# Optimization experiments

Measured on AMD Instinct MI355X. Metric: run time of the kernel, lower is better.

## Reference

```python
import jax, jax.numpy as jnp
import numpy as np

N, E, IN, H, OUT = 50000, 800000, 256, 128, 64


def setup_inputs() -> dict:
    key = jax.random.key(0)
    ks = jax.random.split(key, 4)
    x = jax.random.normal(ks[0], (N, IN), dtype=jnp.float32)
    edge_index = jax.random.randint(ks[1], (2, E), 0, N, dtype=jnp.int64)
    W1 = jax.random.normal(ks[2], (IN, H), dtype=jnp.float32) / np.float32(np.sqrt(IN))
    b1 = jnp.zeros((H,), jnp.float32)
    W2 = jax.random.normal(ks[3], (H, OUT), dtype=jnp.float32) / np.float32(np.sqrt(H))
    b2 = jnp.zeros((OUT,), jnp.float32)
    return {"x": x, "edge_index": edge_index, "W1": W1, "b1": b1, "W2": W2, "b2": b2}


def _gcn_conv(x, W, b, src, dst, norm, n):
    # PyG GCNConv: linear transform, then symmetric-normalized aggregation, then bias
    h = x @ W                                        # [n, d_out]
    agg = jax.ops.segment_sum(h[src] * norm[:, None], dst, num_segments=n)
    return agg + b


def reference(x, edge_index, W1, b1, W2, b2):
    n = x.shape[0]
    loop = jnp.arange(n, dtype=edge_index.dtype)
    # add self-loops (GCNConv default add_self_loops=True)
    src = jnp.concatenate([edge_index[0], loop])
    dst = jnp.concatenate([edge_index[1], loop])
    # symmetric normalization deg^{-1/2} A_hat deg^{-1/2}
    deg = jax.ops.segment_sum(jnp.ones(src.shape, jnp.float32), dst, num_segments=n)
    dinv = jnp.where(deg > 0, jax.lax.rsqrt(deg), 0.0)
    norm = dinv[src] * dinv[dst]                     # [E + n]
    h = jax.nn.relu(_gcn_conv(x, W1, b1, src, dst, norm, n))
    return _gcn_conv(h, W2, b2, src, dst, norm, n)
```

## Files before the change

kernel.cpp:

```cpp
#include <hip/hip_runtime.h>


#define DI 256
#define DH 128
#define DO 64
#define NBC 98
#define EPB 8192
#define P4CAP 12288

typedef unsigned short ushort;
typedef unsigned int uint;
using bf16x8 = __attribute__((ext_vector_type(8))) short;
using f32x4  = __attribute__((ext_vector_type(4))) float;

__device__ __forceinline__ ushort f2b(float f) {
    union { float f; uint u; } v; v.f = f;
    uint r = (v.u + 0x7fffu + ((v.u >> 16) & 1u)) >> 16;
    return (ushort)r;
}
__device__ __forceinline__ float blo(uint v) { return __uint_as_float(v << 16); }
__device__ __forceinline__ float bhi(uint v) { return __uint_as_float(v & 0xffff0000u); }

__global__ __launch_bounds__(256) void hist_k(const int* __restrict__ dst,
                                              int* __restrict__ hist, int E) {
    __shared__ int lh[NBC];
    const int blk = blockIdx.x;
    for (int i = threadIdx.x; i < NBC; i += 256) lh[i] = 0;
    __syncthreads();
    const int base = blk * EPB, end = min(base + EPB, E);
    for (int e = base + threadIdx.x; e < end; e += 256)
        atomicAdd(&lh[dst[e] >> 9], 1);
    __syncthreads();
    for (int i = threadIdx.x; i < NBC; i += 256) hist[blk * NBC + i] = lh[i];
}

__global__ void scan_mat(int* __restrict__ hist, int* __restrict__ boff,
                         int* __restrict__ off, int nbp, int n, int E) {
    __shared__ int mat[NBC * NBC];
    __shared__ int tot[NBC], bo[NBC];
    const int tid = threadIdx.x;
    const int tote = nbp * NBC;
    for (int i = tid; i < tote; i += 256) mat[i] = hist[i];
    __syncthreads();
    if (tid < NBC) {
        int run = 0;
        for (int b = 0; b < nbp; ++b) {
            int v = mat[b * NBC + tid];
            mat[b * NBC + tid] = run;
            run += v;
        }
        tot[tid] = run;
    }
    __syncthreads();
    if (tid == 0) {
        int r = 0;
        for (int c = 0; c < NBC; ++c) { bo[c] = r; r += tot[c]; }
        boff[NBC] = r;
        off[n] = E;
    }
    __syncthreads();
    if (tid < NBC) boff[tid] = bo[tid];
    for (int i = tid; i < tote; i += 256) hist[i] = mat[i] + bo[i % NBC];
}

__global__ __launch_bounds__(256) void part_k(const int* __restrict__ src,
                                              const int* __restrict__ dst,
                                              const int* __restrict__ hist,
                                              uint* __restrict__ pairs, int E) {
    __shared__ int cur[NBC];
    const int blk = blockIdx.x;
    for (int i = threadIdx.x; i < NBC; i += 256) cur[i] = hist[blk * NBC + i];
    __syncthreads();
    const int base = blk * EPB, end = min(base + EPB, E);
    for (int e = base + threadIdx.x; e < end; e += 256) {
        int d = dst[e], s = src[e];
        int slot = atomicAdd(&cur[d >> 9], 1);
        pairs[slot] = ((uint)s << 9) | (uint)(d & 511);
    }
}

__global__ __launch_bounds__(256) void bucket_k(const uint* __restrict__ pairs,
                                                const int* __restrict__ boff,
                                                int* __restrict__ off,
                                                float* __restrict__ dinv,
                                                int* __restrict__ csr, int n) {
    __shared__ int lh[512], lcur[512], tsum[256];
    __shared__ int sorted[P4CAP];
    const int tid = threadIdx.x;
    const int cb = blockIdx.x;
    const int b0 = boff[cb], b1 = boff[cb + 1];
    const int cnt = b1 - b0;
    lh[tid] = 0; lh[tid + 256] = 0;
    __syncthreads();
    for (int i = tid; i < cnt; i += 256) atomicAdd(&lh[pairs[b0 + i] & 511], 1);
    __syncthreads();
    const int s0 = lh[2 * tid], s1 = lh[2 * tid + 1];
    const int s = s0 + s1;
    tsum[tid] = s;
    __syncthreads();
    for (int o = 1; o < 256; o <<= 1) {
        int t = (tid >= o) ? tsum[tid - o] : 0;
        __syncthreads();
        tsum[tid] += t;
        __syncthreads();
    }
    const int ex = tsum[tid] - s;
    lcur[2 * tid] = ex; lcur[2 * tid + 1] = ex + s0;
    {
        int node = cb * 512 + 2 * tid;
        if (node < n)     { off[node]     = b0 + ex;      dinv[node]     = rsqrtf((float)s0 + 1.f); }
        if (node + 1 < n) { off[node + 1] = b0 + ex + s0; dinv[node + 1] = rsqrtf((float)s1 + 1.f); }
    }
    __syncthreads();
    for (int i = tid; i < cnt; i += 256) {
        uint v = pairs[b0 + i];
        int slot = atomicAdd(&lcur[v & 511], 1);
        if (slot < P4CAP) sorted[slot] = (int)(v >> 9);
    }
    __syncthreads();
    const int cs = min(cnt, P4CAP);
    for (int i = tid; i < cs; i += 256) csr[b0 + i] = sorted[i];
}

__global__ void wt_cvt2(const float* __restrict__ W1, ushort* __restrict__ W1t,
                        const float* __restrict__ W2, ushort* __restrict__ W2t) {
    int idx = blockIdx.x * 256 + threadIdx.x;
    if (idx < DI * DH) {
        int m = idx / DI, k = idx % DI;
        W1t[idx] = f2b(W1[(long)k * DH + m]);
    }
    if (idx < DH * DO) {
        int m = idx / DH, k = idx % DH;
        W2t[idx] = f2b(W2[(long)k * DO + m]);
    }
}

template<int K, int M, bool INF32>
__global__ __launch_bounds__(256) void mfma_gemm(const void* __restrict__ Xv,
                                                 const ushort* __restrict__ Wt,
                                                 const float* __restrict__ dinv,
                                                 ushort* __restrict__ Y, int n) {
    constexpr int ROWB = K * 2;
    constexpr int CT = M / 64;
    __shared__ ushort Xs[64 * K];
    const int t = threadIdx.x;
    const int r0 = blockIdx.x * 64;

    {
        const int row = t >> 2, q = t & 3;
        const int gr = r0 + row;
        if (INF32) {
            const float* Xr = (const float*)Xv + (long)gr * K;
#pragma unroll
            for (int j = 0; j < K / 32; ++j) {
                float4 a = make_float4(0.f, 0.f, 0.f, 0.f), b = a;
                if (gr < n) {
                    a = *(const float4*)&Xr[q * 8 + j * 32];
                    b = *(const float4*)&Xr[q * 8 + j * 32 + 4];
                }
                ushort u[8] = {f2b(a.x), f2b(a.y), f2b(a.z), f2b(a.w),
                               f2b(b.x), f2b(b.y), f2b(b.z), f2b(b.w)};
                int byte = row * ROWB + q * 16 + j * 64;
                byte ^= (row & 7) << 4;
                *(uint4*)((char*)Xs + byte) = *(const uint4*)u;
            }
        } else {
            const ushort* Xr = (const ushort*)Xv + (long)gr * K;
#pragma unroll
            for (int j = 0; j < K / 32; ++j) {
                uint4 v = make_uint4(0u, 0u, 0u, 0u);
                if (gr < n) v = *(const uint4*)&Xr[q * 8 + j * 32];
                int byte = row * ROWB + q * 16 + j * 64;
                byte ^= (row & 7) << 4;
                *(uint4*)((char*)Xs + byte) = v;
            }
        }
    }
    __syncthreads();

    const int w  = t >> 6;
    const int l  = t & 63;
    const int lr = l & 15;
    const int lg = l >> 4;
    f32x4 acc[4][CT] = {};

#pragma unroll
    for (int ks = 0; ks < K / 32; ++ks) {
        bf16x8 bfr[CT];
#pragma unroll
        for (int ct = 0; ct < CT; ++ct) {
            int col = w * (M / 4) + ct * 16 + lr;
            bfr[ct] = *(const bf16x8*)&Wt[(long)col * K + ks * 32 + lg * 8];
        }
        bf16x8 afr[4];
#pragma unroll
        for (int rt = 0; rt < 4; ++rt) {
            int row = rt * 16 + lr;
            int byte = row * ROWB + ks * 64 + lg * 16;
            byte ^= (row & 7) << 4;
            afr[rt] = *(const bf16x8*)((const char*)Xs + byte);
        }
#pragma unroll
        for (int rt = 0; rt < 4; ++rt)
#pragma unroll
            for (int ct = 0; ct < CT; ++ct)
                acc[rt][ct] = __builtin_amdgcn_mfma_f32_16x16x32_bf16(
                    afr[rt], bfr[ct], acc[rt][ct], 0, 0, 0);
    }

#pragma unroll
    for (int rt = 0; rt < 4; ++rt)
#pragma unroll
        for (int i = 0; i < 4; ++i) {
            int gr2 = r0 + rt * 16 + lg * 4 + i;
            if (gr2 < n) {
                float dv = dinv[gr2];
#pragma unroll
                for (int ct = 0; ct < CT; ++ct) {
                    int col = w * (M / 4) + ct * 16 + lr;
                    Y[(long)gr2 * M + col] = f2b(dv * acc[rt][ct][i]);
                }
            }
        }
}

template<int M, bool RELU, bool OUTF32>
__global__ __launch_bounds__(256) void gather_wave(const int* __restrict__ off,
                                                   const int* __restrict__ csr,
                                                   const ushort* __restrict__ Hs,
                                                   const float* __restrict__ dinv,
                                                   const float* __restrict__ b,
                                                   void* __restrict__ Yv, int n) {
    constexpr int LPG = M / 8;
    constexpr int GR  = 64 / LPG;
    const int wv = threadIdx.x >> 6;
    const int ln = threadIdx.x & 63;
    const int grp = ln / LPG;
    const int j   = ln % LPG;
    const int i = blockIdx.x * 4 + wv;
    if (i >= n) return;
    const uint4* H4 = (const uint4*)Hs;
    float acc[8] = {0.f, 0.f, 0.f, 0.f, 0.f, 0.f, 0.f, 0.f};
    const int k0 = off[i], ke = off[i + 1];
    for (int k = k0 + grp; k < ke; k += GR) {
        uint4 a = H4[(long)csr[k] * LPG + j];
        acc[0] += blo(a.x); acc[1] += bhi(a.x);
        acc[2] += blo(a.y); acc[3] += bhi(a.y);
        acc[4] += blo(a.z); acc[5] += bhi(a.z);
        acc[6] += blo(a.w); acc[7] += bhi(a.w);
    }
    if (grp == 0) {
        uint4 a = H4[(long)i * LPG + j];
        acc[0] += blo(a.x); acc[1] += bhi(a.x);
        acc[2] += blo(a.y); acc[3] += bhi(a.y);
        acc[4] += blo(a.z); acc[5] += bhi(a.z);
        acc[6] += blo(a.w); acc[7] += bhi(a.w);
    }
#pragma unroll
    for (int o = LPG; o < 64; o <<= 1)
#pragma unroll
        for (int m = 0; m < 8; ++m) acc[m] += __shfl_xor(acc[m], o, 64);
    if (grp == 0) {
        float di = dinv[i];
        float4 b0 = ((const float4*)b)[j * 2];
        float4 b1 = ((const float4*)b)[j * 2 + 1];
        float r[8];
        r[0] = di * acc[0] + b0.x; r[1] = di * acc[1] + b0.y;
        r[2] = di * acc[2] + b0.z; r[3] = di * acc[3] + b0.w;
        r[4] = di * acc[4] + b1.x; r[5] = di * acc[5] + b1.y;
        r[6] = di * acc[6] + b1.z; r[7] = di * acc[7] + b1.w;
        if (RELU) {
#pragma unroll
            for (int m = 0; m < 8; ++m) r[m] = fmaxf(r[m], 0.f);
        }
        if (OUTF32) {
            float* Y = (float*)Yv;
            *(float4*)&Y[(long)i * M + j * 8]     = make_float4(r[0], r[1], r[2], r[3]);
            *(float4*)&Y[(long)i * M + j * 8 + 4] = make_float4(r[4], r[5], r[6], r[7]);
        } else {
            ushort* Y = (ushort*)Yv;
            uint4 o;
            o.x = (uint)f2b(r[0]) | ((uint)f2b(r[1]) << 16);
            o.y = (uint)f2b(r[2]) | ((uint)f2b(r[3]) << 16);
            o.z = (uint)f2b(r[4]) | ((uint)f2b(r[5]) << 16);
            o.w = (uint)f2b(r[6]) | ((uint)f2b(r[7]) << 16);
            *(uint4*)&Y[(long)i * M + j * 8] = o;
        }
    }
}

extern "C" void kernel_launch(void* const* d_in, const int* in_sizes, int n_in,
                              void* d_out, int out_size, void* d_ws, size_t ws_size,
                              hipStream_t stream) {
    const float* x  = (const float*)d_in[0];
    const int*   ei = (const int*)d_in[1];
    const float* W1 = (const float*)d_in[2];
    const float* b1 = (const float*)d_in[3];
    const float* W2 = (const float*)d_in[4];
    const float* b2 = (const float*)d_in[5];
    float* out = (float*)d_out;

    const int n = in_sizes[0] / DI;
    const int E = in_sizes[1] / 2;
    const int* src = ei;
    const int* dst = ei + E;
    const int np  = ((n + 255) / 256) * 256;
    const int nbp = (E + EPB - 1) / EPB;
    const int nbc = (n + 511) >> 9;

    int*    hist  = (int*)d_ws;
    int*    boff  = hist + NBC * NBC;
    int*    off   = boff + 128;
    float*  dinv  = (float*)(off + np + 256);
    int*    csr   = (int*)(dinv + np);
    uint*   pairs = (uint*)(csr + E);
    ushort* w1t   = (ushort*)(pairs + E);
    ushort* w2t   = w1t + DH * DI;
    ushort* h0s   = w2t + DO * DH;
    ushort* h     = h0s + (size_t)n * DH;
    ushort* h1s   = h0s;

    hist_k<<<nbp, 256, 0, stream>>>(dst, hist, E);
    scan_mat<<<1, 256, 0, stream>>>(hist, boff, off, nbp, n, E);
    part_k<<<nbp, 256, 0, stream>>>(src, dst, hist, pairs, E);
    bucket_k<<<nbc, 256, 0, stream>>>(pairs, boff, off, dinv, csr, n);
    wt_cvt2<<<(DI * DH + 255) / 256, 256, 0, stream>>>(W1, w1t, W2, w2t);

    const int gblk = (n + 63) / 64;
    mfma_gemm<DI, DH, true><<<gblk, 256, 0, stream>>>(x, w1t, dinv, h0s, n);
    gather_wave<DH, true, false><<<(n + 3) / 4, 256, 0, stream>>>(off, csr, h0s, dinv, b1, h, n);
    mfma_gemm<DH, DO, false><<<gblk, 256, 0, stream>>>(h, w2t, dinv, h1s, n);
    gather_wave<DO, false, true><<<(n + 3) / 4, 256, 0, stream>>>(off, csr, h1s, dinv, b2, out, n);
}
```

Baseline: 237.9 us.

## Fuse layer-1 aggregation with layer-2 GEMM via shared-memory tile

Adds a gather_gemm kernel in which 1024-thread blocks each aggregate 64 nodes' neighbor features (with bias and ReLU) into a swizzled LDS tile, then multiply that tile by W2 with MFMA and write the scaled layer-2 features. This removes the intermediate hidden-activation round trip through global memory and one kernel launch. The gather loops are also unrolled by two with dual accumulators to get more loads in flight. In exchange, each wave now handles four nodes serially, and the large blocks with heavy LDS use may reduce occupancy and latency hiding in the gather.

```diff
diff --git a/kernel.cpp b/kernel.cpp
--- a/kernel.cpp
+++ b/kernel.cpp
@@ -222,6 +222,101 @@
                 }
             }
         }
+}
+
+__global__ __launch_bounds__(1024, 8) void gather_gemm(const int* __restrict__ off,
+                                                       const int* __restrict__ csr,
+                                                       const ushort* __restrict__ Hs,
+                                                       const float* __restrict__ dinv,
+                                                       const float* __restrict__ b1,
+                                                       const ushort* __restrict__ W2t,
+                                                       ushort* __restrict__ h1s, int n) {
+    __shared__ ushort Xs[64 * DH];
+    const int tid = threadIdx.x;
+    const int wv = tid >> 6, ln = tid & 63;
+    const int grp = ln >> 4, j = ln & 15;
+    const int base = blockIdx.x * 64;
+    const uint4* H4 = (const uint4*)Hs;
+
+#pragma unroll
+    for (int q = 0; q < 4; ++q) {
+        const int row = wv * 4 + q;
+        const int node = base + row;
+        float a0[8] = {}, a1[8] = {};
+        if (node < n) {
+            const int k0 = off[node], ke = off[node + 1];
+            int k = k0 + grp;
+            for (; k + 4 < ke; k += 8) {
+                uint4 va = H4[(long)csr[k] * 16 + j];
+                uint4 vb = H4[(long)csr[k + 4] * 16 + j];
+                a0[0] += blo(va.x); a0[1] += bhi(va.x);
+                a0[2] += blo(va.y); a0[3] += bhi(va.y);
+                a0[4] += blo(va.z); a0[5] += bhi(va.z);
+                a0[6] += blo(va.w); a0[7] += bhi(va.w);
+                a1[0] += blo(vb.x); a1[1] += bhi(vb.x);
+                a1[2] += blo(vb.y); a1[3] += bhi(vb.y);
+                a1[4] += blo(vb.z); a1[5] += bhi(vb.z);
+                a1[6] += blo(vb.w); a1[7] += bhi(vb.w);
+            }
+            if (k < ke) {
+                uint4 va = H4[(long)csr[k] * 16 + j];
+                a0[0] += blo(va.x); a0[1] += bhi(va.x);
+                a0[2] += blo(va.y); a0[3] += bhi(va.y);
+                a0[4] += blo(va.z); a0[5] += bhi(va.z);
+                a0[6] += blo(va.w); a0[7] += bhi(va.w);
+            }
+            if (grp == 0) {
+                uint4 va = H4[(long)node * 16 + j];
+                a1[0] += blo(va.x); a1[1] += bhi(va.x);
+                a1[2] += blo(va.y); a1[3] += bhi(va.y);
+                a1[4] += blo(va.z); a1[5] += bhi(va.z);
+                a1[6] += blo(va.w); a1[7] += bhi(va.w);
+            }
+        }
+        float r[8];
+#pragma unroll
+        for (int m = 0; m < 8; ++m) {
+            r[m] = a0[m] + a1[m];
+            r[m] += __shfl_xor(r[m], 16, 64);
+            r[m] += __shfl_xor(r[m], 32, 64);
+        }
+        if (grp == 0 && node < n) {
+            float di = dinv[node];
+            float4 bb0 = ((const float4*)b1)[j * 2];
+            float4 bb1 = ((const float4*)b1)[j * 2 + 1];
+            ushort u[8];
+            u[0] = f2b(fmaxf(di * r[0] + bb0.x, 0.f));
+            u[1] = f2b(fmaxf(di * r[1] + bb0.y, 0.f));
+            u[2] = f2b(fmaxf(di * r[2] + bb0.z, 0.f));
+            u[3] = f2b(fmaxf(di * r[3] + bb0.w, 0.f));
+            u[4] = f2b(fmaxf(di * r[4] + bb1.x, 0.f));
+            u[5] = f2b(fmaxf(di * r[5] + bb1.y, 0.f));
+            u[6] = f2b(fmaxf(di * r[6] + bb1.z, 0.f));
+            u[7] = f2b(fmaxf(di * r[7] + bb1.w, 0.f));
+            int byte = row * 256 + j * 16;
+            byte ^= (row & 7) << 4;
+            *(uint4*)((char*)Xs + byte) = *(const uint4*)u;
+        }
+    }
+    __syncthreads();
+
+    const int rt = wv >> 2, ct = wv & 3;
+    const int lr = ln & 15, lg = ln >> 4;
+    f32x4 acc = {};
+#pragma unroll
+    for (int ks = 0; ks < 4; ++ks) {
+        bf16x8 bfr = *(const bf16x8*)&W2t[(ct * 16 + lr) * DH + ks * 32 + lg * 8];
+        int rowA = rt * 16 + lr;
+        int byte = rowA * 256 + ks * 64 + lg * 16;
+        byte ^= (rowA & 7) << 4;
+        bf16x8 afr = *(const bf16x8*)((const char*)Xs + byte);
+        acc = __builtin_amdgcn_mfma_f32_16x16x32_bf16(afr, bfr, acc, 0, 0, 0);
+    }
+#pragma unroll
+    for (int i = 0; i < 4; ++i) {
+        int r2 = base + rt * 16 + lg * 4 + i;
+        if (r2 < n) h1s[(long)r2 * DO + ct * 16 + lr] = f2b(dinv[r2] * acc[i]);
+    }
 }
 
 template<int M, bool RELU, bool OUTF32>
@@ -240,26 +335,42 @@
     const int i = blockIdx.x * 4 + wv;
     if (i >= n) return;
     const uint4* H4 = (const uint4*)Hs;
-    float acc[8] = {0.f, 0.f, 0.f, 0.f, 0.f, 0.f, 0.f, 0.f};
+    float a0[8] = {}, a1[8] = {};
     const int k0 = off[i], ke = off[i + 1];
-    for (int k = k0 + grp; k < ke; k += GR) {
-        uint4 a = H4[(long)csr[k] * LPG + j];
-        acc[0] += blo(a.x); acc[1] += bhi(a.x);
-        acc[2] += blo(a.y); acc[3] += bhi(a.y);
-        acc[4] += blo(a.z); acc[5] += bhi(a.z);
-        acc[6] += blo(a.w); acc[7] += bhi(a.w);
+    int k = k0 + grp;
+    for (; k + GR < ke; k += 2 * GR) {
+        uint4 va = H4[(long)csr[k] * LPG + j];
+        uint4 vb = H4[(long)csr[k + GR] * LPG + j];
+        a0[0] += blo(va.x); a0[1] += bhi(va.x);
+        a0[2] += blo(va.y); a0[3] += bhi(va.y);
+        a0[4] += blo(va.z); a0[5] += bhi(va.z);
+        a0[6] += blo(va.w); a0[7] += bhi(va.w);
+        a1[0] += blo(vb.x); a1[1] += bhi(vb.x);
+        a1[2] += blo(vb.y); a1[3] += bhi(vb.y);
+        a1[4] += blo(vb.z); a1[5] += bhi(vb.z);
+        a1[6] += blo(vb.w); a1[7] += bhi(vb.w);
+    }
+    if (k < ke) {
+        uint4 va = H4[(long)csr[k] * LPG + j];
+        a0[0] += blo(va.x); a0[1] += bhi(va.x);
+        a0[2] += blo(va.y); a0[3] += bhi(va.y);
+        a0[4] += blo(va.z); a0[5] += bhi(va.z);
+        a0[6] += blo(va.w); a0[7] += bhi(va.w);
     }
     if (grp == 0) {
-        uint4 a = H4[(long)i * LPG + j];
-        acc[0] += blo(a.x); acc[1] += bhi(a.x);
-        acc[2] += blo(a.y); acc[3] += bhi(a.y);
-        acc[4] += blo(a.z); acc[5] += bhi(a.z);
-        acc[6] += blo(a.w); acc[7] += bhi(a.w);
-    }
-#pragma unroll
-    for (int o = LPG; o < 64; o <<= 1)
-#pragma unroll
-        for (int m = 0; m < 8; ++m) acc[m] += __shfl_xor(acc[m], o, 64);
+        uint4 va = H4[(long)i * LPG + j];
+        a1[0] += blo(va.x); a1[1] += bhi(va.x);
+        a1[2] += blo(va.y); a1[3] += bhi(va.y);
+        a1[4] += blo(va.z); a1[5] += bhi(va.z);
+        a1[6] += blo(va.w); a1[7] += bhi(va.w);
+    }
+    float acc[8];
+#pragma unroll
+    for (int m = 0; m < 8; ++m) {
+        acc[m] = a0[m] + a1[m];
+#pragma unroll
+        for (int o = LPG; o < 64; o <<= 1) acc[m] += __shfl_xor(acc[m], o, 64);
+    }
     if (grp == 0) {
         float di = dinv[i];
         float4 b0 = ((const float4*)b)[j * 2];
@@ -317,8 +428,7 @@
     ushort* w1t   = (ushort*)(pairs + E);
     ushort* w2t   = w1t + DH * DI;
     ushort* h0s   = w2t + DO * DH;
-    ushort* h     = h0s + (size_t)n * DH;
-    ushort* h1s   = h0s;
+    ushort* h1s   = h0s + (size_t)n * DH;
 
     hist_k<<<nbp, 256, 0, stream>>>(dst, hist, E);
     scan_mat<<<1, 256, 0, stream>>>(hist, boff, off, nbp, n, E);
@@ -328,7 +438,6 @@
 
     const int gblk = (n + 63) / 64;
     mfma_gemm<DI, DH, true><<<gblk, 256, 0, stream>>>(x, w1t, dinv, h0s, n);
-    gather_wave<DH, true, false><<<(n + 3) / 4, 256, 0, stream>>>(off, csr, h0s, dinv, b1, h, n);
-    mfma_gemm<DH, DO, false><<<gblk, 256, 0, stream>>>(h, w2t, dinv, h1s, n);
+    gather_gemm<<<gblk, 1024, 0, stream>>>(off, csr, h0s, dinv, b1, w2t, h1s, n);
     gather_wave<DO, false, true><<<(n + 3) / 4, 256, 0, stream>>>(off, csr, h1s, dinv, b2, out, n);
 }
```

Measured after the change: 232.9 us. -2.1%, faster.

## Split layer-1 gather into column halves, unroll gathers, fold weight conversion into hist

Applied to the files above, without the earlier changes.

The layer-1 gather now splits each node's 128 columns across two blocks, so eight edge groups work in parallel per wave, each keeping two independent accumulators. The layer-2 gather unrolls by four with separate accumulators to keep more loads in flight. Weight transpose/conversion is folded into the histogram kernel to remove one launch. The h1s buffer no longer aliases h0s. Splitting the columns re-reads the csr indices twice and doubles the block count, and the hard-coded stride 25088 assumes nbp*256 threads cover the W1 indices.

```diff
diff --git a/kernel.cpp b/kernel.cpp
--- a/kernel.cpp
+++ b/kernel.cpp
@@ -22,11 +22,28 @@
 __device__ __forceinline__ float bhi(uint v) { return __uint_as_float(v & 0xffff0000u); }
 
 __global__ __launch_bounds__(256) void hist_k(const int* __restrict__ dst,
-                                              int* __restrict__ hist, int E) {
+                                              int* __restrict__ hist, int E,
+                                              const float* __restrict__ W1,
+                                              ushort* __restrict__ W1t,
+                                              const float* __restrict__ W2,
+                                              ushort* __restrict__ W2t) {
     __shared__ int lh[NBC];
     const int blk = blockIdx.x;
     for (int i = threadIdx.x; i < NBC; i += 256) lh[i] = 0;
     __syncthreads();
+    const int gid = blk * 256 + threadIdx.x;
+#pragma unroll
+    for (int r = 0; r < 2; ++r) {
+        int idx = gid + r * 25088;
+        if (idx < DI * DH) {
+            int m = idx / DI, k = idx % DI;
+            W1t[idx] = f2b(W1[(long)k * DH + m]);
+        }
+    }
+    if (gid < DH * DO) {
+        int m = gid / DH, k = gid % DH;
+        W2t[gid] = f2b(W2[(long)k * DO + m]);
+    }
     const int base = blk * EPB, end = min(base + EPB, E);
     for (int e = base + threadIdx.x; e < end; e += 256)
         atomicAdd(&lh[dst[e] >> 9], 1);
@@ -120,19 +137,6 @@
     __syncthreads();
     const int cs = min(cnt, P4CAP);
     for (int i = tid; i < cs; i += 256) csr[b0 + i] = sorted[i];
-}
-
-__global__ void wt_cvt2(const float* __restrict__ W1, ushort* __restrict__ W1t,
-                        const float* __restrict__ W2, ushort* __restrict__ W2t) {
-    int idx = blockIdx.x * 256 + threadIdx.x;
-    if (idx < DI * DH) {
-        int m = idx / DI, k = idx % DI;
-        W1t[idx] = f2b(W1[(long)k * DH + m]);
-    }
-    if (idx < DH * DO) {
-        int m = idx / DH, k = idx % DH;
-        W2t[idx] = f2b(W2[(long)k * DO + m]);
-    }
 }
 
 template<int K, int M, bool INF32>
@@ -224,68 +228,130 @@
         }
 }
 
-template<int M, bool RELU, bool OUTF32>
-__global__ __launch_bounds__(256) void gather_wave(const int* __restrict__ off,
+__global__ __launch_bounds__(256) void gather_half(const int* __restrict__ off,
                                                    const int* __restrict__ csr,
                                                    const ushort* __restrict__ Hs,
                                                    const float* __restrict__ dinv,
-                                                   const float* __restrict__ b,
-                                                   void* __restrict__ Yv, int n) {
-    constexpr int LPG = M / 8;
-    constexpr int GR  = 64 / LPG;
-    const int wv = threadIdx.x >> 6;
-    const int ln = threadIdx.x & 63;
-    const int grp = ln / LPG;
-    const int j   = ln % LPG;
+                                                   const float* __restrict__ b1,
+                                                   ushort* __restrict__ h, int n) {
+    const int wv = threadIdx.x >> 6, ln = threadIdx.x & 63;
+    const int grp = ln >> 3, j = ln & 7;
+    const int half = blockIdx.x & 1;
+    const int i = (blockIdx.x >> 1) * 4 + wv;
+    if (i >= n) return;
+    const uint4* H4 = (const uint4*)Hs;
+    const int cb = half * 8 + j;
+    float a0[8] = {}, a1[8] = {};
+    const int k0 = off[i], ke = off[i + 1];
+    int k = k0 + grp;
+    for (; k + 8 < ke; k += 16) {
+        uint4 va = H4[(long)csr[k] * 16 + cb];
+        uint4 vb = H4[(long)csr[k + 8] * 16 + cb];
+        a0[0] += blo(va.x); a0[1] += bhi(va.x);
+        a0[2] += blo(va.y); a0[3] += bhi(va.y);
+        a0[4] += blo(va.z); a0[5] += bhi(va.z);
+        a0[6] += blo(va.w); a0[7] += bhi(va.w);
+        a1[0] += blo(vb.x); a1[1] += bhi(vb.x);
+        a1[2] += blo(vb.y); a1[3] += bhi(vb.y);
+        a1[4] += blo(vb.z); a1[5] += bhi(vb.z);
+        a1[6] += blo(vb.w); a1[7] += bhi(vb.w);
+    }
+    if (k < ke) {
+        uint4 va = H4[(long)csr[k] * 16 + cb];
+        a0[0] += blo(va.x); a0[1] += bhi(va.x);
+        a0[2] += blo(va.y); a0[3] += bhi(va.y);
+        a0[4] += blo(va.z); a0[5] += bhi(va.z);
+        a0[6] += blo(va.w); a0[7] += bhi(va.w);
+    }
+    if (grp == 0) {
+        uint4 va = H4[(long)i * 16 + cb];
+        a1[0] += blo(va.x); a1[1] += bhi(va.x);
+        a1[2] += blo(va.y); a1[3] += bhi(va.y);
+        a1[4] += blo(va.z); a1[5] += bhi(va.z);
+        a1[6] += blo(va.w); a1[7] += bhi(va.w);
+    }
+    float acc[8];
+#pragma unroll
+    for (int m = 0; m < 8; ++m) {
+        acc[m] = a0[m] + a1[m];
+        acc[m] += __shfl_xor(acc[m], 8, 64);
+        acc[m] += __shfl_xor(acc[m], 16, 64);
+        acc[m] += __shfl_xor(acc[m], 32, 64);
+    }
+    if (grp == 0) {
+        float di = dinv[i];
+        float4 bb0 = ((const float4*)b1)[cb * 2];
+        float4 bb1 = ((const float4*)b1)[cb * 2 + 1];
+        ushort u[8];
+        u[0] = f2b(fmaxf(di * acc[0] + bb0.x, 0.f));
+        u[1] = f2b(fmaxf(di * acc[1] + bb0.y, 0.f));
+        u[2] = f2b(fmaxf(di * acc[2] + bb0.z, 0.f));
+        u[3] = f2b(fmaxf(di * acc[3] + bb0.w, 0.f));
+        u[4] = f2b(fmaxf(di * acc[4] + bb1.x, 0.f));
+        u[5] = f2b(fmaxf(di * acc[5] + bb1.y, 0.f));
+        u[6] = f2b(fmaxf(di * acc[6] + bb1.z, 0.f));
+        u[7] = f2b(fmaxf(di * acc[7] + bb1.w, 0.f));
+        *(uint4*)&h[(long)i * DH + cb * 8] = *(const uint4*)u;
+    }
+}
+
+__global__ __launch_bounds__(256) void gather_out(const int* __restrict__ off,
+                                                  const int* __restrict__ csr,
+                                                  const ushort* __restrict__ Hs,
+                                                  const float* __restrict__ dinv,
+                                                  const float* __restrict__ b,
+                                                  float* __restrict__ Y, int n) {
+    const int wv = threadIdx.x >> 6, ln = threadIdx.x & 63;
+    const int grp = ln >> 3, j = ln & 7;
     const int i = blockIdx.x * 4 + wv;
     if (i >= n) return;
     const uint4* H4 = (const uint4*)Hs;
-    float acc[8] = {0.f, 0.f, 0.f, 0.f, 0.f, 0.f, 0.f, 0.f};
+    float a0[8] = {}, a1[8] = {}, a2[8] = {}, a3[8] = {};
     const int k0 = off[i], ke = off[i + 1];
-    for (int k = k0 + grp; k < ke; k += GR) {
-        uint4 a = H4[(long)csr[k] * LPG + j];
-        acc[0] += blo(a.x); acc[1] += bhi(a.x);
-        acc[2] += blo(a.y); acc[3] += bhi(a.y);
-        acc[4] += blo(a.z); acc[5] += bhi(a.z);
-        acc[6] += blo(a.w); acc[7] += bhi(a.w);
+    int k = k0 + grp;
+    for (; k + 24 < ke; k += 32) {
+        uint4 va = H4[(long)csr[k]      * 8 + j];
+        uint4 vb = H4[(long)csr[k + 8]  * 8 + j];
+        uint4 vc = H4[(long)csr[k + 16] * 8 + j];
+        uint4 vd = H4[(long)csr[k + 24] * 8 + j];
+        a0[0] += blo(va.x); a0[1] += bhi(va.x); a0[2] += blo(va.y); a0[3] += bhi(va.y);
+        a0[4] += blo(va.z); a0[5] += bhi(va.z); a0[6] += blo(va.w); a0[7] += bhi(va.w);
+        a1[0] += blo(vb.x); a1[1] += bhi(vb.x); a1[2] += blo(vb.y); a1[3] += bhi(vb.y);
+        a1[4] += blo(vb.z); a1[5] += bhi(vb.z); a1[6] += blo(vb.w); a1[7] += bhi(vb.w);
+        a2[0] += blo(vc.x); a2[1] += bhi(vc.x); a2[2] += blo(vc.y); a2[3] += bhi(vc.y);
+        a2[4] += blo(vc.z); a2[5] += bhi(vc.z); a2[6] += blo(vc.w); a2[7] += bhi(vc.w);
+        a3[0] += blo(vd.x); a3[1] += bhi(vd.x); a3[2] += blo(vd.y); a3[3] += bhi(vd.y);
+        a3[4] += blo(vd.z); a3[5] += bhi(vd.z); a3[6] += blo(vd.w); a3[7] += bhi(vd.w);
+    }
+    for (; k < ke; k += 8) {
+        uint4 va = H4[(long)csr[k] * 8 + j];
+        a0[0] += blo(va.x); a0[1] += bhi(va.x); a0[2] += blo(va.y); a0[3] += bhi(va.y);
+        a0[4] += blo(va.z); a0[5] += bhi(va.z); a0[6] += blo(va.w); a0[7] += bhi(va.w);
     }
     if (grp == 0) {
-        uint4 a = H4[(long)i * LPG + j];
-        acc[0] += blo(a.x); acc[1] += bhi(a.x);
-        acc[2] += blo(a.y); acc[3] += bhi(a.y);
-        acc[4] += blo(a.z); acc[5] += bhi(a.z);
-        acc[6] += blo(a.w); acc[7] += bhi(a.w);
-    }
-#pragma unroll
-    for (int o = LPG; o < 64; o <<= 1)
-#pragma unroll
-        for (int m = 0; m < 8; ++m) acc[m] += __shfl_xor(acc[m], o, 64);
+        uint4 va = H4[(long)i * 8 + j];
+        a1[0] += blo(va.x); a1[1] += bhi(va.x); a1[2] += blo(va.y); a1[3] += bhi(va.y);
+        a1[4] += blo(va.z); a1[5] += bhi(va.z); a1[6] += blo(va.w); a1[7] += bhi(va.w);
+    }
+    float acc[8];
+#pragma unroll
+    for (int m = 0; m < 8; ++m) {
+        acc[m] = (a0[m] + a1[m]) + (a2[m] + a3[m]);
+        acc[m] += __shfl_xor(acc[m], 8, 64);
+        acc[m] += __shfl_xor(acc[m], 16, 64);
+        acc[m] += __shfl_xor(acc[m], 32, 64);
+    }
     if (grp == 0) {
         float di = dinv[i];
         float4 b0 = ((const float4*)b)[j * 2];
         float4 b1 = ((const float4*)b)[j * 2 + 1];
-        float r[8];
-        r[0] = di * acc[0] + b0.x; r[1] = di * acc[1] + b0.y;
-        r[2] = di * acc[2] + b0.z; r[3] = di * acc[3] + b0.w;
-        r[4] = di * acc[4] + b1.x; r[5] = di * acc[5] + b1.y;
-        r[6] = di * acc[6] + b1.z; r[7] = di * acc[7] + b1.w;
-        if (RELU) {
-#pragma unroll
-            for (int m = 0; m < 8; ++m) r[m] = fmaxf(r[m], 0.f);
-        }
-        if (OUTF32) {
-            float* Y = (float*)Yv;
-            *(float4*)&Y[(long)i * M + j * 8]     = make_float4(r[0], r[1], r[2], r[3]);
-            *(float4*)&Y[(long)i * M + j * 8 + 4] = make_float4(r[4], r[5], r[6], r[7]);
-        } else {
-            ushort* Y = (ushort*)Yv;
-            uint4 o;
-            o.x = (uint)f2b(r[0]) | ((uint)f2b(r[1]) << 16);
-            o.y = (uint)f2b(r[2]) | ((uint)f2b(r[3]) << 16);
-            o.z = (uint)f2b(r[4]) | ((uint)f2b(r[5]) << 16);
-            o.w = (uint)f2b(r[6]) | ((uint)f2b(r[7]) << 16);
-            *(uint4*)&Y[(long)i * M + j * 8] = o;
-        }
+        float4 o0, o1;
+        o0.x = di * acc[0] + b0.x; o0.y = di * acc[1] + b0.y;
+        o0.z = di * acc[2] + b0.z; o0.w = di * acc[3] + b0.w;
+        o1.x = di * acc[4] + b1.x; o1.y = di * acc[5] + b1.y;
+        o1.z = di * acc[6] + b1.z; o1.w = di * acc[7] + b1.w;
+        *(float4*)&Y[(long)i * DO + j * 8]     = o0;
+        *(float4*)&Y[(long)i * DO + j * 8 + 4] = o1;
     }
 }
 
@@ -318,17 +384,16 @@
     ushort* w2t   = w1t + DH * DI;
     ushort* h0s   = w2t + DO * DH;
     ushort* h     = h0s + (size_t)n * DH;
-    ushort* h1s   = h0s;
-
-    hist_k<<<nbp, 256, 0, stream>>>(dst, hist, E);
+    ushort* h1s   = h + (size_t)n * DH;
+
+    hist_k<<<nbp, 256, 0, stream>>>(dst, hist, E, W1, w1t, W2, w2t);
     scan_mat<<<1, 256, 0, stream>>>(hist, boff, off, nbp, n, E);
     part_k<<<nbp, 256, 0, stream>>>(src, dst, hist, pairs, E);
     bucket_k<<<nbc, 256, 0, stream>>>(pairs, boff, off, dinv, csr, n);
-    wt_cvt2<<<(DI * DH + 255) / 256, 256, 0, stream>>>(W1, w1t, W2, w2t);
 
     const int gblk = (n + 63) / 64;
     mfma_gemm<DI, DH, true><<<gblk, 256, 0, stream>>>(x, w1t, dinv, h0s, n);
-    gather_wave<DH, true, false><<<(n + 3) / 4, 256, 0, stream>>>(off, csr, h0s, dinv, b1, h, n);
+    gather_half<<<2 * ((n + 3) / 4), 256, 0, stream>>>(off, csr, h0s, dinv, b1, h, n);
     mfma_gemm<DH, DO, false><<<gblk, 256, 0, stream>>>(h, w2t, dinv, h1s, n);
-    gather_wave<DO, false, true><<<(n + 3) / 4, 256, 0, stream>>>(off, csr, h1s, dinv, b2, out, n);
-}
+    gather_out<<<(n + 3) / 4, 256, 0, stream>>>(off, csr, h1s, dinv, b2, out, n);
+}
```

After: 252.2 us. 1.06x slower.
